# Optimization experiments

Hardware: AMD Instinct MI355X
Metric: run time of the kernel (lower is better)

Reference implementation:

```python
import jax, jax.numpy as jnp
import numpy as np

N, E, D_IN, D_HID, D_OUT = 100000, 1600000, 128, 128, 40

def _sage_pool(x, src, dst, Wp, bp, Ws, Wn, b, n_nodes):
    # DGL SAGEConv 'pool': h_pool = relu(fc_pool(x)); h_neigh = max over in-neighbors;
    # out = fc_self(x) + fc_neigh(h_neigh) + bias
    hp = jax.nn.relu(x @ Wp + bp)                       # [N, d]
    msg = hp[src]                                        # [E, d] gather
    agg = jax.ops.segment_max(msg, dst, num_segments=n_nodes)  # [N, d] scatter-max
    agg = jnp.where(jnp.isfinite(agg), agg, 0.0)         # zero-in-degree nodes -> 0
    return x @ Ws + agg @ Wn + b

def setup_inputs() -> dict:
    key = jax.random.key(0)
    ks = jax.random.split(key, 14)
    def lin(k, i, o):
        return jax.random.normal(k, (i, o), dtype=jnp.float32) / np.sqrt(i)
    return {
        "in_feat": jax.random.normal(ks[0], (N, D_IN), dtype=jnp.float32),
        "src": jax.random.randint(ks[1], (E,), 0, N),
        "dst": jax.random.randint(ks[2], (E,), 0, N),
        "Wp1": lin(ks[3], D_IN, D_IN), "bp1": jnp.zeros((D_IN,), jnp.float32),
        "Ws1": lin(ks[4], D_IN, D_HID), "Wn1": lin(ks[5], D_IN, D_HID),
        "b1": jnp.zeros((D_HID,), jnp.float32),
        "Wp2": lin(ks[6], D_HID, D_HID), "bp2": jnp.zeros((D_HID,), jnp.float32),
        "Ws2": lin(ks[7], D_HID, D_OUT), "Wn2": lin(ks[8], D_HID, D_OUT),
        "b2": jnp.zeros((D_OUT,), jnp.float32),
    }

def reference(in_feat, src, dst, Wp1, bp1, Ws1, Wn1, b1, Wp2, bp2, Ws2, Wn2, b2):
    h = _sage_pool(in_feat, src, dst, Wp1, bp1, Ws1, Wn1, b1, N)
    h = jax.nn.relu(h)
    # dropout is identity at inference (eval mode)
    return _sage_pool(h, src, dst, Wp2, bp2, Ws2, Wn2, b2, N)
```

## Files before the change

### kernel.cpp

```cpp
#include <hip/hip_runtime.h>
#include <stdint.h>

#define NN 100000
#define NE 1600000
#define NB 196

using u16 = unsigned short;
using u32 = unsigned int;

typedef __attribute__((ext_vector_type(8))) short bf16x8;
typedef __attribute__((ext_vector_type(4))) float f32x4;

__device__ inline u16 f2b(float f){
  u32 u = __float_as_uint(f);
  u32 r = (u + 0x7fffu + ((u >> 16) & 1u)) >> 16;
  return (u16)r;
}

__device__ inline bf16x8 cvt8(const float* __restrict__ p){
  float4 a = *(const float4*)p;
  float4 b = *(const float4*)(p + 4);
  union { u32 w[4]; bf16x8 v; } u;
  u.w[0] = (u32)f2b(a.x) | ((u32)f2b(a.y) << 16);
  u.w[1] = (u32)f2b(a.z) | ((u32)f2b(a.w) << 16);
  u.w[2] = (u32)f2b(b.x) | ((u32)f2b(b.y) << 16);
  u.w[3] = (u32)f2b(b.z) | ((u32)f2b(b.w) << 16);
  return u.v;
}

__global__ void k_prep(const float* __restrict__ Wp1, const float* __restrict__ Ws1,
                       const float* __restrict__ Wn1, const float* __restrict__ Wp2,
                       const float* __restrict__ Ws2, const float* __restrict__ Wn2,
                       u16* __restrict__ wpT1, u16* __restrict__ wc1T,
                       u16* __restrict__ wpT2, u16* __restrict__ wc2T,
                       int* __restrict__ cb){
  int i = blockIdx.x * 256 + threadIdx.x;
  if (i < NB) cb[i] = 0;
  if (i < 16384){ int n = i >> 7, k = i & 127;
    wpT1[n*128 + k] = f2b(Wp1[k*128 + n]);
    wpT2[n*128 + k] = f2b(Wp2[k*128 + n]);
  }
  if (i < 32768){ int n = i >> 8, k = i & 255;
    float v = (k < 128) ? Ws1[k*128 + n] : Wn1[(k-128)*128 + n];
    wc1T[n*256 + k] = f2b(v);
  }
  if (i < 12288){ int n = i >> 8, k = i & 255;
    float v = 0.f;
    if (n < 40) v = (k < 128) ? Ws2[k*40 + n] : Wn2[(k-128)*40 + n];
    wc2T[n*256 + k] = f2b(v);
  }
}

__global__ __launch_bounds__(256) void k_cb_hist(const int* __restrict__ dst,
                                                 int* __restrict__ cb){
  __shared__ int h[NB];
  for (int i = threadIdx.x; i < NB; i += 256) h[i] = 0;
  __syncthreads();
  int e0 = blockIdx.x * 8192;
  #pragma unroll 4
  for (int j = 0; j < 32; j++){
    int e = e0 + j * 256 + threadIdx.x;
    if (e < NE) atomicAdd(&h[dst[e] >> 9], 1);
  }
  __syncthreads();
  for (int i = threadIdx.x; i < NB; i += 256)
    if (h[i]) atomicAdd(&cb[i], h[i]);
}

__global__ __launch_bounds__(256) void k_cb_scan(const int* __restrict__ cb,
                                                 int* __restrict__ cbo,
                                                 int* __restrict__ curB){
  __shared__ int s[256];
  int tid = threadIdx.x;
  int v = (tid < NB) ? cb[tid] : 0;
  s[tid] = v;
  __syncthreads();
  #pragma unroll
  for (int off = 1; off < 256; off <<= 1){
    int t = (tid >= off) ? s[tid - off] : 0;
    __syncthreads();
    s[tid] += t;
    __syncthreads();
  }
  int ex = s[tid] - v;
  if (tid < NB){ cbo[tid] = ex; curB[tid] = ex; }
  if (tid == 255) cbo[NB] = s[255];
}

__global__ __launch_bounds__(256) void k_part(const int* __restrict__ src,
                                              const int* __restrict__ dst,
                                              int* __restrict__ curB,
                                              int2* __restrict__ part){
  __shared__ int hist[256], scn[256], cur[256], base[256];
  __shared__ int2 stage[4096];
  const int tid = threadIdx.x;
  const int e0 = blockIdx.x * 4096;
  const int cnt = min(4096, NE - e0);
  hist[tid] = 0;
  __syncthreads();
  int2 ed[16];
  #pragma unroll
  for (int j = 0; j < 16; j++){
    int e = e0 + j * 256 + tid;
    if (e < NE){
      ed[j].x = src[e]; ed[j].y = dst[e];
      atomicAdd(&hist[ed[j].y >> 9], 1);
    }
  }
  __syncthreads();
  int hv = hist[tid];
  base[tid] = (tid < NB && hv) ? atomicAdd(&curB[tid], hv) : 0;
  scn[tid] = hv;
  __syncthreads();
  #pragma unroll
  for (int off = 1; off < 256; off <<= 1){
    int t = (tid >= off) ? scn[tid - off] : 0;
    __syncthreads();
    scn[tid] += t;
    __syncthreads();
  }
  int ex = scn[tid] - hv;
  scn[tid] = ex;
  cur[tid] = ex;
  __syncthreads();
  #pragma unroll
  for (int j = 0; j < 16; j++){
    int e = e0 + j * 256 + tid;
    if (e < NE){
      int slot = atomicAdd(&cur[ed[j].y >> 9], 1);
      stage[slot] = ed[j];
    }
  }
  __syncthreads();
  for (int i = tid; i < cnt; i += 256){
    int2 p = stage[i];
    int b = p.y >> 9;
    part[base[b] + (i - scn[b])] = p;
  }
}

__global__ __launch_bounds__(512) void k_bsort(const int2* __restrict__ part,
                                               const int* __restrict__ cbo,
                                               int* __restrict__ rp,
                                               int* __restrict__ esrc){
  __shared__ int cnt[512], sc[512], cur[512];
  const int tid = threadIdx.x;
  const int b = blockIdx.x;
  const int lo = cbo[b], hi = cbo[b + 1];
  cnt[tid] = 0;
  __syncthreads();
  for (int i = lo + tid; i < hi; i += 512)
    atomicAdd(&cnt[part[i].y & 511], 1);
  __syncthreads();
  sc[tid] = cnt[tid];
  __syncthreads();
  #pragma unroll
  for (int off = 1; off < 512; off <<= 1){
    int t = (tid >= off) ? sc[tid - off] : 0;
    __syncthreads();
    sc[tid] += t;
    __syncthreads();
  }
  int ex = sc[tid] - cnt[tid];
  int n = (b << 9) + tid;
  if (n < NN) rp[n] = lo + ex;
  if (b == NB - 1 && tid == 0) rp[NN] = hi;
  cur[tid] = lo + ex;
  __syncthreads();
  for (int i = lo + tid; i < hi; i += 512){
    int2 p = part[i];
    int pos = atomicAdd(&cur[p.y & 511], 1);
    esrc[pos] = p.x;
  }
}

__global__ void k_agg(const u16* __restrict__ hp, const int* __restrict__ rp,
                      const int* __restrict__ esrc, u16* __restrict__ agg){
  int node = blockIdx.x * 4 + (threadIdx.x >> 6);
  if (node >= NN) return;
  const int lane = threadIdx.x & 63;
  const int half = lane >> 5;
  const int l32  = lane & 31;
  const int lo = rp[node], hi = rp[node + 1];
  u32 m0 = 0, m1 = 0;
  for (int i = lo; i < hi; i += 16){
    int s[8];
    #pragma unroll
    for (int j = 0; j < 8; j++){
      int ii = i + 2 * j + half; if (ii >= hi) ii = hi - 1;
      s[j] = esrc[ii];
    }
    uint2 v[8];
    #pragma unroll
    for (int j = 0; j < 8; j++)
      v[j] = *(const uint2*)&hp[(size_t)s[j] * 128 + l32 * 4];
    #pragma unroll
    for (int j = 0; j < 8; j++){
      asm("v_pk_max_u16 %0, %0, %1" : "+v"(m0) : "v"(v[j].x));
      asm("v_pk_max_u16 %0, %0, %1" : "+v"(m1) : "v"(v[j].y));
    }
  }
  u32 t0 = (u32)__shfl_xor((int)m0, 32);
  u32 t1 = (u32)__shfl_xor((int)m1, 32);
  asm("v_pk_max_u16 %0, %0, %1" : "+v"(m0) : "v"(t0));
  asm("v_pk_max_u16 %0, %0, %1" : "+v"(m1) : "v"(t1));
  if (half == 0)
    *(uint2*)&agg[(size_t)node * 128 + l32 * 4] = make_uint2(m0, m1);
}

template<int K, int NOUT, int NOUTR, bool A1F32, bool HASA2, bool RELU, bool OUTF32>
__global__ __launch_bounds__(512)
void k_dgemm(const void* __restrict__ A1p, const u16* __restrict__ A2,
             const u16* __restrict__ Wt, const float* __restrict__ bias,
             void* __restrict__ outp)
{
  constexpr int KP  = K + 8;
  constexpr int NTI = NOUT / 16;
  __shared__ u16 W_lds[NOUT * KP];
  const int tid  = threadIdx.x;
  const int row0 = blockIdx.x * 128;
  const int wave = tid >> 6, lane = tid & 63;
  const int colb = lane & 15;
  const int koff = (lane >> 4) * 8;

  for (int c = tid; c < NOUT * (K / 8); c += 512){
    int n = c / (K / 8), kc = c % (K / 8);
    *(uint4*)&W_lds[n * KP + kc * 8] = *(const uint4*)&Wt[n * K + kc * 8];
  }
  __syncthreads();

  const int rowl = wave * 16 + colb;
  const int rA   = min(row0 + rowl, NN - 1);

  f32x4 acc[NTI] = {};

  #pragma unroll
  for (int k0 = 0; k0 < K; k0 += 64){
    bf16x8 af0, af1;
    if (A1F32 && k0 < 128){
      const float* A = (const float*)A1p;
      af0 = cvt8(&A[(size_t)rA * 128 + k0 + koff]);
      af1 = cvt8(&A[(size_t)rA * 128 + k0 + 32 + koff]);
    } else {
      const u16* A = (HASA2 && k0 >= 128) ? A2 : (const u16*)A1p;
      int kb = (HASA2 && k0 >= 128) ? (k0 - 128) : k0;
      af0 = *(const bf16x8*)&A[(size_t)rA * 128 + kb + koff];
      af1 = *(const bf16x8*)&A[(size_t)rA * 128 + kb + 32 + koff];
    }
    #pragma unroll
    for (int nt = 0; nt < NTI; nt++){
      const u16* Wr = &W_lds[(nt * 16 + colb) * KP + k0];
      bf16x8 b0 = *(const bf16x8*)&Wr[koff];
      bf16x8 b1 = *(const bf16x8*)&Wr[32 + koff];
      acc[nt] = __builtin_amdgcn_mfma_f32_16x16x32_bf16(af0, b0, acc[nt], 0, 0, 0);
      acc[nt] = __builtin_amdgcn_mfma_f32_16x16x32_bf16(af1, b1, acc[nt], 0, 0, 0);
    }
  }

  const int rowc = wave * 16 + ((lane >> 4) << 2);
  #pragma unroll
  for (int nt = 0; nt < NTI; nt++){
    int col = nt * 16 + colb;
    if (col >= NOUTR) continue;
    float bv = bias[col];
    #pragma unroll
    for (int r = 0; r < 4; r++){
      int gr = row0 + rowc + r;
      if (gr >= NN) continue;
      float v = acc[nt][r] + bv;
      if (RELU) v = fmaxf(v, 0.f);
      if (OUTF32) ((float*)outp)[(size_t)gr * NOUTR + col] = v;
      else        ((u16*)outp)[(size_t)gr * NOUTR + col] = f2b(v);
    }
  }
}

extern "C" void kernel_launch(void* const* d_in, const int* in_sizes, int n_in,
                              void* d_out, int out_size, void* d_ws, size_t ws_size,
                              hipStream_t stream){
  const float* x   = (const float*)d_in[0];
  const int*   src = (const int*)d_in[1];
  const int*   dst = (const int*)d_in[2];
  const float* Wp1 = (const float*)d_in[3];
  const float* bp1 = (const float*)d_in[4];
  const float* Ws1 = (const float*)d_in[5];
  const float* Wn1 = (const float*)d_in[6];
  const float* b1  = (const float*)d_in[7];
  const float* Wp2 = (const float*)d_in[8];
  const float* bp2 = (const float*)d_in[9];
  const float* Ws2 = (const float*)d_in[10];
  const float* Wn2 = (const float*)d_in[11];
  const float* b2  = (const float*)d_in[12];

  char* ws = (char*)d_ws;
  u16* wpT1 = (u16*)(ws + 0);
  u16* wc1T = (u16*)(ws + 32768);
  u16* wpT2 = (u16*)(ws + 98304);
  u16* wc2T = (u16*)(ws + 131072);
  int* cb   = (int*)(ws + 155648);
  int* cbo  = (int*)(ws + 157696);
  int* curB = (int*)(ws + 159744);
  int* rp   = (int*)(ws + 161792);
  int2* part= (int2*)(ws + 561920);
  u16* h    = (u16*)(ws + 561920);
  int* esrc = (int*)(ws + 26161920);
  u16* hp   = (u16*)(ws + 32561920);
  u16* agg  = (u16*)(ws + 58161920);

  k_prep<<<128, 256, 0, stream>>>(Wp1, Ws1, Wn1, Wp2, Ws2, Wn2,
                                  wpT1, wc1T, wpT2, wc2T, cb);
  k_cb_hist<<<(NE + 8191) / 8192, 256, 0, stream>>>(dst, cb);
  k_cb_scan<<<1, 256, 0, stream>>>(cb, cbo, curB);
  k_part<<<(NE + 4095) / 4096, 256, 0, stream>>>(src, dst, curB, part);
  k_bsort<<<NB, 512, 0, stream>>>(part, cbo, rp, esrc);

  k_dgemm<128,128,128, true ,false,true ,false>
      <<<(NN + 127) / 128, 512, 0, stream>>>(x, nullptr, wpT1, bp1, hp);
  k_agg<<<(NN + 3) / 4, 256, 0, stream>>>(hp, rp, esrc, agg);
  k_dgemm<256,128,128, true ,true ,true ,false>
      <<<(NN + 127) / 128, 512, 0, stream>>>(x, agg, wc1T, b1, h);
  k_dgemm<128,128,128, false,false,true ,false>
      <<<(NN + 127) / 128, 512, 0, stream>>>(h, nullptr, wpT2, bp2, hp);
  k_agg<<<(NN + 3) / 4, 256, 0, stream>>>(hp, rp, esrc, agg);
  k_dgemm<256, 48, 40, false,true ,false,true >
      <<<(NN + 127) / 128, 512, 0, stream>>>(h, agg, wc2T, b2, d_out);
}
```

Before: 251.8 us.

## Use finer CSR buckets, pack partitioned edges into 32-bit words, retune launches

The two-pass counting sort that builds the CSR now uses 256-node buckets (391 buckets) instead of 512-node ones, so there are twice as many k_bsort blocks for better GPU occupancy. Partitioned edges are packed into a single u32 (local dst in the high bits, src in the low 17 bits) instead of an int2, which halves the intermediate traffic. Histogram and partition kernels get larger blocks with fewer edges per thread. The risks are the 17-bit src packing limit and the extra partition scan work over more buckets.

After: 251.0 us. No clear change (-0.3%).

```diff
diff --git a/kernel.cpp b/kernel.cpp
--- a/kernel.cpp
+++ b/kernel.cpp
@@ -3,7 +3,7 @@
 
 #define NN 100000
 #define NE 1600000
-#define NB 196
+#define NB 391
 
 using u16 = unsigned short;
 using u32 = unsigned int;
@@ -51,32 +51,32 @@
   }
 }
 
-__global__ __launch_bounds__(256) void k_cb_hist(const int* __restrict__ dst,
+__global__ __launch_bounds__(512) void k_cb_hist(const int* __restrict__ dst,
                                                  int* __restrict__ cb){
   __shared__ int h[NB];
-  for (int i = threadIdx.x; i < NB; i += 256) h[i] = 0;
-  __syncthreads();
-  int e0 = blockIdx.x * 8192;
-  #pragma unroll 4
-  for (int j = 0; j < 32; j++){
-    int e = e0 + j * 256 + threadIdx.x;
-    if (e < NE) atomicAdd(&h[dst[e] >> 9], 1);
-  }
-  __syncthreads();
-  for (int i = threadIdx.x; i < NB; i += 256)
+  for (int i = threadIdx.x; i < NB; i += 512) h[i] = 0;
+  __syncthreads();
+  int e0 = blockIdx.x * 2048 + threadIdx.x;
+  #pragma unroll
+  for (int j = 0; j < 4; j++){
+    int e = e0 + j * 512;
+    if (e < NE) atomicAdd(&h[dst[e] >> 8], 1);
+  }
+  __syncthreads();
+  for (int i = threadIdx.x; i < NB; i += 512)
     if (h[i]) atomicAdd(&cb[i], h[i]);
 }
 
-__global__ __launch_bounds__(256) void k_cb_scan(const int* __restrict__ cb,
+__global__ __launch_bounds__(512) void k_cb_scan(const int* __restrict__ cb,
                                                  int* __restrict__ cbo,
                                                  int* __restrict__ curB){
-  __shared__ int s[256];
+  __shared__ int s[512];
   int tid = threadIdx.x;
   int v = (tid < NB) ? cb[tid] : 0;
   s[tid] = v;
   __syncthreads();
   #pragma unroll
-  for (int off = 1; off < 256; off <<= 1){
+  for (int off = 1; off < 512; off <<= 1){
     int t = (tid >= off) ? s[tid - off] : 0;
     __syncthreads();
     s[tid] += t;
@@ -84,93 +84,90 @@
   }
   int ex = s[tid] - v;
   if (tid < NB){ cbo[tid] = ex; curB[tid] = ex; }
-  if (tid == 255) cbo[NB] = s[255];
-}
-
-__global__ __launch_bounds__(256) void k_part(const int* __restrict__ src,
-                                              const int* __restrict__ dst,
-                                              int* __restrict__ curB,
-                                              int2* __restrict__ part){
-  __shared__ int hist[256], scn[256], cur[256], base[256];
+  if (tid == 511) cbo[NB] = s[511];
+}
+
+__global__ __launch_bounds__(1024) void k_part(const int* __restrict__ src,
+                                               const int* __restrict__ dst,
+                                               int* __restrict__ curB,
+                                               u32* __restrict__ part){
+  __shared__ int hist[NB], scn[NB], cur[NB], base[NB];
   __shared__ int2 stage[4096];
   const int tid = threadIdx.x;
   const int e0 = blockIdx.x * 4096;
   const int cnt = min(4096, NE - e0);
-  hist[tid] = 0;
-  __syncthreads();
-  int2 ed[16];
-  #pragma unroll
-  for (int j = 0; j < 16; j++){
-    int e = e0 + j * 256 + tid;
+  for (int i = tid; i < NB; i += 1024) hist[i] = 0;
+  __syncthreads();
+  int2 ed[4];
+  #pragma unroll
+  for (int j = 0; j < 4; j++){
+    int e = e0 + j * 1024 + tid;
     if (e < NE){
       ed[j].x = src[e]; ed[j].y = dst[e];
-      atomicAdd(&hist[ed[j].y >> 9], 1);
-    }
-  }
-  __syncthreads();
-  int hv = hist[tid];
-  base[tid] = (tid < NB && hv) ? atomicAdd(&curB[tid], hv) : 0;
-  scn[tid] = hv;
-  __syncthreads();
-  #pragma unroll
-  for (int off = 1; off < 256; off <<= 1){
-    int t = (tid >= off) ? scn[tid - off] : 0;
-    __syncthreads();
-    scn[tid] += t;
-    __syncthreads();
-  }
-  int ex = scn[tid] - hv;
-  scn[tid] = ex;
-  cur[tid] = ex;
-  __syncthreads();
-  #pragma unroll
-  for (int j = 0; j < 16; j++){
-    int e = e0 + j * 256 + tid;
+      atomicAdd(&hist[ed[j].y >> 8], 1);
+    }
+  }
+  __syncthreads();
+  int hv = (tid < NB) ? hist[tid] : 0;
+  if (tid < NB) base[tid] = hv ? atomicAdd(&curB[tid], hv) : 0;
+  #pragma unroll
+  for (int off = 1; off < 512; off <<= 1){
+    int t = 0;
+    if (tid < 512 && tid >= off && tid - off < NB) t = hist[tid - off];
+    __syncthreads();
+    if (tid < NB) hist[tid] += t;
+    __syncthreads();
+  }
+  if (tid < NB){ int ex = hist[tid] - hv; scn[tid] = ex; cur[tid] = ex; }
+  __syncthreads();
+  #pragma unroll
+  for (int j = 0; j < 4; j++){
+    int e = e0 + j * 1024 + tid;
     if (e < NE){
-      int slot = atomicAdd(&cur[ed[j].y >> 9], 1);
+      int slot = atomicAdd(&cur[ed[j].y >> 8], 1);
       stage[slot] = ed[j];
     }
   }
   __syncthreads();
-  for (int i = tid; i < cnt; i += 256){
+  for (int i = tid; i < cnt; i += 1024){
     int2 p = stage[i];
-    int b = p.y >> 9;
-    part[base[b] + (i - scn[b])] = p;
-  }
-}
-
-__global__ __launch_bounds__(512) void k_bsort(const int2* __restrict__ part,
+    int b = p.y >> 8;
+    part[base[b] + (i - scn[b])] = ((u32)(p.y & 255) << 17) | (u32)p.x;
+  }
+}
+
+__global__ __launch_bounds__(256) void k_bsort(const u32* __restrict__ part,
                                                const int* __restrict__ cbo,
                                                int* __restrict__ rp,
                                                int* __restrict__ esrc){
-  __shared__ int cnt[512], sc[512], cur[512];
+  __shared__ int cnt[256], sc[256], cur[256];
   const int tid = threadIdx.x;
   const int b = blockIdx.x;
   const int lo = cbo[b], hi = cbo[b + 1];
   cnt[tid] = 0;
   __syncthreads();
-  for (int i = lo + tid; i < hi; i += 512)
-    atomicAdd(&cnt[part[i].y & 511], 1);
+  for (int i = lo + tid; i < hi; i += 256)
+    atomicAdd(&cnt[part[i] >> 17], 1);
   __syncthreads();
   sc[tid] = cnt[tid];
   __syncthreads();
   #pragma unroll
-  for (int off = 1; off < 512; off <<= 1){
+  for (int off = 1; off < 256; off <<= 1){
     int t = (tid >= off) ? sc[tid - off] : 0;
     __syncthreads();
     sc[tid] += t;
     __syncthreads();
   }
   int ex = sc[tid] - cnt[tid];
-  int n = (b << 9) + tid;
+  int n = (b << 8) + tid;
   if (n < NN) rp[n] = lo + ex;
   if (b == NB - 1 && tid == 0) rp[NN] = hi;
   cur[tid] = lo + ex;
   __syncthreads();
-  for (int i = lo + tid; i < hi; i += 512){
-    int2 p = part[i];
-    int pos = atomicAdd(&cur[p.y & 511], 1);
-    esrc[pos] = p.x;
+  for (int i = lo + tid; i < hi; i += 256){
+    u32 p = part[i];
+    int pos = atomicAdd(&cur[p >> 17], 1);
+    esrc[pos] = (int)(p & 0x1FFFFu);
   }
 }
 
@@ -301,7 +298,7 @@
   int* cbo  = (int*)(ws + 157696);
   int* curB = (int*)(ws + 159744);
   int* rp   = (int*)(ws + 161792);
-  int2* part= (int2*)(ws + 561920);
+  u32* part = (u32*)(ws + 561920);
   u16* h    = (u16*)(ws + 561920);
   int* esrc = (int*)(ws + 26161920);
   u16* hp   = (u16*)(ws + 32561920);
@@ -309,10 +306,10 @@
 
   k_prep<<<128, 256, 0, stream>>>(Wp1, Ws1, Wn1, Wp2, Ws2, Wn2,
                                   wpT1, wc1T, wpT2, wc2T, cb);
-  k_cb_hist<<<(NE + 8191) / 8192, 256, 0, stream>>>(dst, cb);
-  k_cb_scan<<<1, 256, 0, stream>>>(cb, cbo, curB);
-  k_part<<<(NE + 4095) / 4096, 256, 0, stream>>>(src, dst, curB, part);
-  k_bsort<<<NB, 512, 0, stream>>>(part, cbo, rp, esrc);
+  k_cb_hist<<<(NE + 2047) / 2048, 512, 0, stream>>>(dst, cb);
+  k_cb_scan<<<1, 512, 0, stream>>>(cb, cbo, curB);
+  k_part<<<(NE + 4095) / 4096, 1024, 0, stream>>>(src, dst, curB, part);
+  k_bsort<<<NB, 256, 0, stream>>>(part, cbo, rp, esrc);
 
   k_dgemm<128,128,128, true ,false,true ,false>
       <<<(NN + 127) / 128, 512, 0, stream>>>(x, nullptr, wpT1, bp1, hp);
```
